# Performance work log

Hardware: AMD Instinct MI355X
Metric: run time of the kernel (lower is better)

The kernel has to match this reference:

```python
import jax, jax.numpy as jnp
import numpy as np

N_NODES = 32768
N_EDGES = 262144
EMB = 64
NUM_HEADS = 4
FEATURE_FDIM = 9
B_MOL = 2048
MAX_PER_MOL = 32


def setup_inputs() -> dict:
    key = jax.random.key(0)
    ks = list(jax.random.split(key, 32))
    nk = lambda: ks.pop()
    inp = {}
    inp['node_feats'] = jax.random.normal(nk(), (N_NODES, FEATURE_FDIM), jnp.float32)
    inp['feature_dist_graph'] = jax.random.normal(nk(), (N_EDGES, FEATURE_FDIM), jnp.float32)
    inp['rij_dist_pairs'] = jax.random.uniform(nk(), (N_EDGES,), jnp.float32)
    see = jax.random.randint(nk(), (N_EDGES, 2), 1, N_NODES + 1, dtype=jnp.int32)
    inp['start_end_env'] = see
    inp['b_scope'] = see[:, 1]  # destination node per edge (index 0 = pad row, never used)
    inp['scope_update'] = jax.random.randint(nk(), (N_EDGES,), 1, N_NODES + 1, dtype=jnp.int32)
    inp['scope_update_lig'] = jax.random.randint(nk(), (N_EDGES,), 1, N_NODES + 1, dtype=jnp.int32)
    inp['l_scope'] = jax.random.randint(nk(), (B_MOL, MAX_PER_MOL), 0, N_NODES + 1, dtype=jnp.int32)
    s = 0.1
    inp['W_emb'] = jax.random.normal(nk(), (FEATURE_FDIM, EMB), jnp.float32) * s
    inp['b_emb'] = jnp.zeros((EMB,), jnp.float32)
    inp['W_dist'] = jax.random.normal(nk(), (FEATURE_FDIM + 1, EMB), jnp.float32) * s
    inp['b_dist'] = jnp.zeros((EMB,), jnp.float32)
    for i in range(NUM_HEADS - 1):
        d = EMB * (i + 1)
        inp[f'fc_W{i}'] = jax.random.normal(nk(), (d, d), jnp.float32) * (1.0 / np.sqrt(d))
        inp[f'fc_b{i}'] = jnp.zeros((d,), jnp.float32)
        inp[f'attn_a{i}'] = jax.random.normal(nk(), (2 * EMB + d, 1), jnp.float32) * s
    return inp


def _segment_attend(logits, vals, seg, num_seg):
    # segment-wise softmax over edges, then weighted scatter-sum to nodes
    m = jax.ops.segment_max(logits, seg, num_segments=num_seg)
    ex = jnp.exp(logits - m[seg])
    den = jax.ops.segment_sum(ex, seg, num_segments=num_seg)
    alpha = ex / den[seg]
    return jax.ops.segment_sum(alpha[:, None] * vals, seg, num_segments=num_seg)


def _forward(node_feats, feature_dist_graph, rij_dist_pairs,
             start_end_env, b_scope, scope_update, scope_update_lig, l_scope,
             W_emb, b_emb, W_dist, b_dist, fc_Ws, fc_bs, attn_as):
    h_orig = node_feats @ W_emb + b_emb                       # [N, EMB]
    h_orig = jnp.concatenate([jnp.zeros((1, EMB), h_orig.dtype), h_orig], axis=0)  # pad row 0
    msg_in = jnp.concatenate([feature_dist_graph, rij_dist_pairs[:, None]], axis=1)
    message = msg_in @ W_dist + b_dist                        # [E, EMB]
    num_seg = h_orig.shape[0]
    tf_feats = h_orig
    for i in range(NUM_HEADS - 1):
        nbr = h_orig[start_end_env]                           # gather: [E, 2, EMB]
        h = message @ fc_Ws[i] + fc_bs[i]                     # [E, D_i]
        logits = jax.nn.leaky_relu(
            jnp.concatenate([nbr[:, 0], nbr[:, 1], h], axis=1) @ attn_as[i],
            negative_slope=0.2)[:, 0]                         # [E]
        out = jax.nn.elu(_segment_attend(logits, h, b_scope, num_seg))  # [N+1, D_i]
        tf_feats = jnp.concatenate([out, h_orig], axis=1)     # merge='cat' -> D_i + EMB
        # updateConnectedDict: rebuild per-edge messages from updated node features
        message = 0.5 * (tf_feats[scope_update_lig] + tf_feats[scope_update])
    cmp_enc = tf_feats[l_scope]                               # [B, P, NUM_HEADS*EMB]
    return cmp_enc.sum(axis=1)                                # [B, NUM_HEADS*EMB]


def reference(node_feats, feature_dist_graph, rij_dist_pairs,
              start_end_env, b_scope, scope_update, scope_update_lig, l_scope,
              W_emb, b_emb, W_dist, b_dist,
              fc_W0, fc_b0, attn_a0, fc_W1, fc_b1, attn_a1, fc_W2, fc_b2, attn_a2):
    return _forward(node_feats, feature_dist_graph, rij_dist_pairs,
                    start_end_env, b_scope, scope_update, scope_update_lig, l_scope,
                    W_emb, b_emb, W_dist, b_dist,
                    [fc_W0, fc_W1, fc_W2], [fc_b0, fc_b1, fc_b2],
                    [attn_a0, attn_a1, attn_a2])
```

## Files before the change

kernel.cpp:

```cpp
#include <hip/hip_runtime.h>
#include <cstdint>
#include <cstddef>

#define NSEG 32769
#define NNODES 32768
#define NE 262144
#define PSZ ((size_t)NSEG * 64)

using f4 = float4;
typedef __attribute__((ext_vector_type(8))) short bf16x8;
typedef __attribute__((ext_vector_type(4))) float f32x4;

__device__ ushort g_tfp[4 * PSZ];
__device__ uint   g_pkA[PSZ];
__device__ uint   g_pk01[PSZ];
__device__ ushort g_msumh[(size_t)NSEG * 192];
__device__ float  g_q[NSEG];
__device__ float  g_p0[3][NSEG];
__device__ float  g_p1[3][NSEG];
__device__ float  g_w2[3][256];
__device__ float  g_wq10[10];
__device__ float  g_cq;
__device__ float  g_wc[640];
__device__ float  g_bcc[64];
__device__ ushort g_wbB[16384];
__device__ ushort g_wbC[36864];
__device__ int    g_counts[NSEG];
__device__ int    g_excl[NSEG];
__device__ int    g_bsum[1024];
__device__ int    g_rowptr[NSEG + 1];
__device__ int    g_cur[NSEG];
__device__ int    g_csr[NE];
__device__ int    g_g1s[NE];
__device__ int    g_g2s[NE];
__device__ float  g_pe1[NE];
__device__ float  g_pe2[NE];
__device__ int    g_bc[128];
__device__ int    g_bcur[128];
__device__ int    g_sorder[NSEG];

#define WREDUCE(x) { x += __shfl_xor(x, 32); x += __shfl_xor(x, 16); \
                     x += __shfl_xor(x, 8);  x += __shfl_xor(x, 4);  \
                     x += __shfl_xor(x, 2);  x += __shfl_xor(x, 1); }
#define WREDMAX(x) { x = fmaxf(x, __shfl_xor(x, 32)); x = fmaxf(x, __shfl_xor(x, 16)); \
                     x = fmaxf(x, __shfl_xor(x, 8));  x = fmaxf(x, __shfl_xor(x, 4));  \
                     x = fmaxf(x, __shfl_xor(x, 2));  x = fmaxf(x, __shfl_xor(x, 1)); }

__device__ __forceinline__ ushort f2bf(float x) {
    uint u = __float_as_uint(x);
    u += 0x7FFF + ((u >> 16) & 1);
    return (ushort)(u >> 16);
}
__device__ __forceinline__ float bfs(ushort u) { return __uint_as_float(((uint)u) << 16); }
__device__ __forceinline__ float bflo(uint u) { return __uint_as_float(u << 16); }
__device__ __forceinline__ float bfhi(uint u) { return __uint_as_float(u & 0xFFFF0000u); }

__global__ __launch_bounds__(256) void k_front(
    const float* __restrict__ node_feats, const float* __restrict__ We,
    const float* __restrict__ be,
    const float* __restrict__ a0, const float* __restrict__ a1, const float* __restrict__ a2,
    const float* __restrict__ W0, const float* __restrict__ W1, const float* __restrict__ W2,
    const float* __restrict__ b0, const float* __restrict__ b1, const float* __restrict__ b2,
    const float* __restrict__ Wd, const float* __restrict__ bd,
    const int* __restrict__ bscope) {
    int tid = threadIdx.x;
    if (blockIdx.x < 513) {
        __shared__ float Ws[576];
        __shared__ float As6[6][68];
        __shared__ float fsAll[576];
        __shared__ float hsAll[64][68];
        int r0 = blockIdx.x * 64;
        for (int i = tid; i < 576; i += 256) Ws[i] = We[i];
        for (int t = tid; t < 384; t += 256) {
            int vec = t >> 6, j = t & 63;
            const float* Av = (vec >> 1) == 0 ? a0 : ((vec >> 1) == 1 ? a1 : a2);
            As6[vec][j] = Av[((vec & 1) << 6) + j];
        }
        for (int t = tid; t < 576; t += 256) {
            int row = r0 + t / 9;
            float v = 0.f;
            if (row >= 1 && row <= NNODES) v = node_feats[(size_t)(row - 1) * 9 + (t % 9)];
            fsAll[t] = v;
        }
        __syncthreads();
        int j = tid & 63;
        float bj = be[j];
#pragma unroll 4
        for (int p = 0; p < 16; p++) {
            int lr = p * 4 + (tid >> 6);
            int row = r0 + lr;
            float acc = bj;
#pragma unroll
            for (int k = 0; k < 9; k++) acc += fsAll[lr * 9 + k] * Ws[k * 64 + j];
            float v = (row == 0 || row >= NSEG) ? 0.f : acc;
            if (row < NSEG) g_tfp[3 * PSZ + (size_t)row * 64 + j] = f2bf(v);
            hsAll[lr][j] = v;
        }
        __syncthreads();
#pragma unroll
        for (int i = 0; i < 12; i++) {
            int task = i * 256 + tid;
            int d = task >> 3, g = tid & 7;
            int lr = d / 6, vec = d % 6;
            float s = 0.f;
#pragma unroll
            for (int jj = 0; jj < 8; jj++)
                s += hsAll[lr][g * 8 + jj] * As6[vec][g * 8 + jj];
            s += __shfl_xor(s, 1); s += __shfl_xor(s, 2); s += __shfl_xor(s, 4);
            int prow = r0 + lr;
            if (g == 0 && prow < NSEG) {
                int iv = vec >> 1;
                if ((vec & 1) == 0) g_p0[iv][prow] = s;
                else                g_p1[iv][prow] = s;
            }
        }
    } else if (blockIdx.x < 518) {
        int pb = blockIdx.x - 513;
        int k = tid;
        if (pb < 3) {
            int it = pb;
            const float* W = it == 0 ? W0 : (it == 1 ? W1 : W2);
            const float* a = it == 0 ? a0 : (it == 1 ? a1 : a2);
            const float* bias = it == 0 ? b0 : (it == 1 ? b1 : b2);
            int d = 64 * (it + 1);
            if (k < d) {
                float s = 0.f;
                for (int jj = 0; jj < d; jj++) s += W[(size_t)k * d + jj] * a[128 + jj];
                g_w2[it][k] = s;
            } else if (k == 255) {
                float c = 0.f;
                for (int jj = 0; jj < d; jj++) c += a[128 + jj] * bias[jj];
                g_w2[it][255] = c;
            }
        } else if (pb == 3) {
            __shared__ float w2s[64];
            if (k < 64) {
                float s = 0.f;
                for (int jj = 0; jj < 64; jj++) s += W0[(size_t)k * 64 + jj] * a0[128 + jj];
                w2s[k] = s;
            }
            __syncthreads();
            if (k < 10) {
                float s = 0.f;
                for (int jj = 0; jj < 64; jj++) s += Wd[(size_t)k * 64 + jj] * w2s[jj];
                g_wq10[k] = s;
            } else if (k == 64) {
                float s = 0.f, c = 0.f;
                for (int jj = 0; jj < 64; jj++) { s += bd[jj] * w2s[jj]; c += a0[128 + jj] * b0[jj]; }
                g_cq = s + c;
            }
        } else {
            for (int t = k; t < 640; t += 256) {
                int kk = t >> 6, jj = t & 63;
                float s = 0.f;
                for (int m = 0; m < 64; m++) s += Wd[kk * 64 + m] * W0[(size_t)m * 64 + jj];
                g_wc[t] = s;
            }
            if (k < 64) {
                float s = b0[k];
                for (int m = 0; m < 64; m++) s += bd[m] * W0[(size_t)m * 64 + k];
                g_bcc[k] = s;
            }
        }
    } else if (blockIdx.x == 518) {
        for (int t = tid; t < 2048; t += 256) {
            int nt = t >> 8, ks = (t >> 6) & 3, l = t & 63;
            int n = nt * 16 + (l & 15);
            int kb = ks * 32 + ((l >> 4) << 3);
            ushort* dst = &g_wbB[(size_t)t * 8];
#pragma unroll
            for (int i = 0; i < 8; i++)
                dst[i] = f2bf(W1[(size_t)(kb + i) * 128 + n]);
        }
    } else if (blockIdx.x <= 520) {
        int half = blockIdx.x - 519;
        for (int t = tid; t < 2304; t += 256) {
            int nt = half * 6 + t / 384;
            int rem = t % 384;
            int ks = rem >> 6, l = rem & 63;
            int n = nt * 16 + (l & 15);
            int kb = ks * 32 + ((l >> 4) << 3);
            ushort* dst = &g_wbC[((size_t)(nt * 6 + ks) * 64 + l) * 8];
#pragma unroll
            for (int i = 0; i < 8; i++)
                dst[i] = f2bf(W2[(size_t)(kb + i) * 192 + n]);
        }
    } else {
        int e = (blockIdx.x - 521) * 256 + tid;
        if (e < NE) atomicAdd(&g_counts[bscope[e]], 1);
    }
}

__global__ void k_scan1() {
    __shared__ int s[256];
    int t = threadIdx.x, i = blockIdx.x * 256 + t;
    int v = (i < NSEG) ? g_counts[i] : 0;
    s[t] = v; __syncthreads();
    for (int off = 1; off < 256; off <<= 1) {
        int tmp = (t >= off) ? s[t - off] : 0;
        __syncthreads();
        s[t] += tmp;
        __syncthreads();
    }
    if (i < NSEG) g_excl[i] = s[t] - v;
    if (t == 255) g_bsum[blockIdx.x] = s[255];
}

__global__ void k_scan2(int nb) {
    __shared__ int s[256];
    int t = threadIdx.x;
    int v = (t < nb) ? g_bsum[t] : 0;
    s[t] = v; __syncthreads();
    for (int off = 1; off < 256; off <<= 1) {
        int tmp = (t >= off) ? s[t - off] : 0;
        __syncthreads();
        s[t] += tmp;
        __syncthreads();
    }
    if (t < nb) g_bsum[t] = s[t] - v;
}

__global__ void k_scan3() {
    __shared__ int lh[128];
    int t = threadIdx.x;
    if (t < 128) lh[t] = 0;
    __syncthreads();
    int i = blockIdx.x * 256 + t;
    if (i < NSEG) {
        g_rowptr[i] = g_excl[i] + g_bsum[i >> 8];
        int cnt = g_counts[i];
        atomicAdd(&lh[cnt > 127 ? 127 : cnt], 1);
    }
    if (i == NSEG) g_rowptr[NSEG] = NE;
    __syncthreads();
    if (t < 128 && lh[t]) atomicAdd(&g_bc[t], lh[t]);
}

__global__ void k_scatter(const int* __restrict__ bs) {
    int e = blockIdx.x * 256 + threadIdx.x;
    if (e < NE) {
        int seg = bs[e];
        int pos = g_rowptr[seg] + atomicAdd(&g_cur[seg], 1);
        g_csr[pos] = e;
    }
}

__global__ __launch_bounds__(256) void k_mid(const int* __restrict__ g1,
                                             const int* __restrict__ g2,
                                             const int* __restrict__ see,
                                             const float* __restrict__ fdg,
                                             const float* __restrict__ rij) {
    int tid = threadIdx.x;
    if (blockIdx.x < 129) {
        __shared__ int sc[128];
        __shared__ int lh[128];
        __shared__ int lbase[128];
        if (tid < 128) { sc[tid] = g_bc[tid]; lh[tid] = 0; }
        __syncthreads();
        for (int off = 1; off < 128; off <<= 1) {
            int tmp = (tid >= off && tid < 128) ? sc[tid - off] : 0;
            __syncthreads();
            if (tid < 128) sc[tid] += tmp;
            __syncthreads();
        }
        int seg = blockIdx.x * 256 + tid;
        int bin = 0, lpos = 0;
        bool valid = seg < NSEG;
        if (valid) {
            int cnt = g_rowptr[seg + 1] - g_rowptr[seg];
            bin = cnt > 127 ? 127 : cnt;
            lpos = atomicAdd(&lh[bin], 1);
        }
        __syncthreads();
        if (tid < 128 && lh[tid] > 0)
            lbase[tid] = atomicAdd(&g_bcur[tid], lh[tid]);
        __syncthreads();
        if (valid) {
            int bstart = sc[bin] - g_bc[bin];
            g_sorder[bstart + lbase[bin] + lpos] = seg;
            g_counts[seg] = 0;
            g_cur[seg] = 0;
        }
    } else if (blockIdx.x < 1153) {
        int pos = (blockIdx.x - 129) * 256 + tid;
        if (pos >= NE) return;
        int e = g_csr[pos];
        g_g1s[pos] = g1[e]; g_g2s[pos] = g2[e];
        int s0 = see[2 * (size_t)e], s1 = see[2 * (size_t)e + 1];
        g_pe1[pos] = g_p0[1][s0] + g_p1[1][s1];
        g_pe2[pos] = g_p0[2][s0] + g_p1[2][s1];
    } else {
        __shared__ float Wcs[640];
        __shared__ float bcs[64];
        __shared__ float wqs[10];
        for (int i = tid; i < 640; i += 256) Wcs[i] = g_wc[i];
        if (tid < 64) bcs[tid] = g_bcc[tid];
        if (tid < 10) wqs[tid] = g_wq10[tid];
        __syncthreads();
        float cq = g_cq;
        int lane = tid & 63;
        int seg = (blockIdx.x - 1153) * 4 + (tid >> 6);
        if (seg >= NSEG) return;
        int beg = g_rowptr[seg], end = g_rowptr[seg + 1];
        int cnt = end - beg;
        float y[10];
#pragma unroll
        for (int k = 0; k < 10; k++) y[k] = 0.f;

        if (cnt > 0 && cnt <= 64) {
            float l = -1e30f;
            float x[10];
#pragma unroll
            for (int k = 0; k < 10; k++) x[k] = 0.f;
            if (lane < cnt) {
                int e = g_csr[beg + lane];
#pragma unroll
                for (int k = 0; k < 9; k++) x[k] = fdg[(size_t)e * 9 + k];
                x[9] = rij[e];
                int s0 = see[2 * (size_t)e], s1 = see[2 * (size_t)e + 1];
                float q = cq;
#pragma unroll
                for (int k = 0; k < 10; k++) q += x[k] * wqs[k];
                l = q + g_p0[0][s0] + g_p1[0][s1];
                l = l > 0.f ? l : 0.2f * l;
            }
            float m = l;
            WREDMAX(m);
            float ex = (lane < cnt) ? __expf(l - m) : 0.f;
            float den = ex;
            WREDUCE(den);
            float w = ex / den;
#pragma unroll
            for (int k = 0; k < 10; k++) {
                float s = w * x[k];
                WREDUCE(s);
                y[k] = s;
            }
        } else if (cnt > 64) {
            float m = -1e30f;
            for (int t = beg + lane; t < end; t += 64) {
                int e = g_csr[t];
                float q = cq;
#pragma unroll
                for (int k = 0; k < 9; k++) q += fdg[(size_t)e * 9 + k] * wqs[k];
                q += rij[e] * wqs[9];
                float l = q + g_p0[0][see[2 * (size_t)e]] + g_p1[0][see[2 * (size_t)e + 1]];
                l = l > 0.f ? l : 0.2f * l;
                m = fmaxf(m, l);
            }
            WREDMAX(m);
            float den = 0.f;
            for (int t = beg + lane; t < end; t += 64) {
                int e = g_csr[t];
                float q = cq;
#pragma unroll
                for (int k = 0; k < 9; k++) q += fdg[(size_t)e * 9 + k] * wqs[k];
                q += rij[e] * wqs[9];
                float l = q + g_p0[0][see[2 * (size_t)e]] + g_p1[0][see[2 * (size_t)e + 1]];
                l = l > 0.f ? l : 0.2f * l;
                den += __expf(l - m);
            }
            WREDUCE(den);
            float rden = 1.f / den;
            float part[10];
#pragma unroll
            for (int k = 0; k < 10; k++) part[k] = 0.f;
            for (int t = beg + lane; t < end; t += 64) {
                int e = g_csr[t];
                float x[10];
#pragma unroll
                for (int k = 0; k < 9; k++) x[k] = fdg[(size_t)e * 9 + k];
                x[9] = rij[e];
                float q = cq;
#pragma unroll
                for (int k = 0; k < 10; k++) q += x[k] * wqs[k];
                float l = q + g_p0[0][see[2 * (size_t)e]] + g_p1[0][see[2 * (size_t)e + 1]];
                l = l > 0.f ? l : 0.2f * l;
                float w = __expf(l - m) * rden;
#pragma unroll
                for (int k = 0; k < 10; k++) part[k] += w * x[k];
            }
#pragma unroll
            for (int k = 0; k < 10; k++) {
                WREDUCE(part[k]);
                y[k] = part[k];
            }
        }
        float o = bcs[lane];
#pragma unroll
        for (int k = 0; k < 10; k++) o += y[k] * Wcs[k * 64 + lane];
        if (cnt == 0) o = 0.f;
        o = o > 0.f ? o : (__expf(o) - 1.f);
        ushort h = g_tfp[3 * PSZ + (size_t)seg * 64 + lane];
        g_pkA[(size_t)seg * 64 + lane] = (uint)f2bf(o) | ((uint)h << 16);
        float qp = o * g_w2[1][lane] + bfs(h) * g_w2[1][64 + lane];
        WREDUCE(qp);
        if (lane == 0) g_q[seg] = qp + g_w2[1][255];
    }
}

template <int NCM>
__global__ __launch_bounds__(256) void k_attendG() {
    const float* __restrict__ pe = (NCM == 2) ? g_pe1 : g_pe2;
    int lane = threadIdx.x & 63;
    int sidx = blockIdx.x * 4 + (threadIdx.x >> 6);
    if (sidx >= NSEG) return;
    int seg = g_sorder[sidx];
    int beg = g_rowptr[seg], end = g_rowptr[seg + 1];
    int cnt = end - beg;
    float acc[NCM];
#pragma unroll
    for (int c = 0; c < NCM; c++) acc[c] = 0.f;

    if (cnt > 0 && cnt <= 64) {
        float l = -1e30f;
        int i1 = 0, i2 = 0;
        if (lane < cnt) {
            i1 = g_g1s[beg + lane]; i2 = g_g2s[beg + lane];
            l = 0.5f * (g_q[i1] + g_q[i2]) + pe[beg + lane];
            l = l > 0.f ? l : 0.2f * l;
        }
        float m = l;
        WREDMAX(m);
        float ex = (lane < cnt) ? __expf(l - m) : 0.f;
        float den = ex;
        WREDUCE(den);
        float w = ex / den;
        for (int t0 = 0; t0 < cnt; t0 += 8) {
            float wt[8]; int a1[8], a2[8];
#pragma unroll
            for (int u = 0; u < 8; u++) {
                int su = t0 + u; su = su > 63 ? 63 : su;
                wt[u] = __shfl(w, su);
                a1[u] = __shfl(i1, su);
                a2[u] = __shfl(i2, su);
            }
            if (NCM == 2) {
                uint ua[8], ub[8];
#pragma unroll
                for (int u = 0; u < 8; u++) {
                    ua[u] = g_pkA[(size_t)a1[u] * 64 + lane];
                    ub[u] = g_pkA[(size_t)a2[u] * 64 + lane];
                }
#pragma unroll
                for (int u = 0; u < 8; u++) {
                    float wh = 0.5f * wt[u];
                    acc[0] += wh * (bflo(ua[u]) + bflo(ub[u]));
                    acc[1] += wh * (bfhi(ua[u]) + bfhi(ub[u]));
                }
            } else {
                uint ua[8], ub[8];
                ushort ha[8], hb[8];
#pragma unroll
                for (int u = 0; u < 8; u++) {
                    size_t b1 = (size_t)a1[u] * 64 + lane, b2 = (size_t)a2[u] * 64 + lane;
                    ua[u] = g_pk01[b1]; ub[u] = g_pk01[b2];
                    ha[u] = g_tfp[3 * PSZ + b1]; hb[u] = g_tfp[3 * PSZ + b2];
                }
#pragma unroll
                for (int u = 0; u < 8; u++) {
                    float wh = 0.5f * wt[u];
                    acc[0] += wh * (bflo(ua[u]) + bflo(ub[u]));
                    acc[1] += wh * (bfhi(ua[u]) + bfhi(ub[u]));
                    acc[2] += wh * (bfs(ha[u]) + bfs(hb[u]));
                }
            }
        }
    } else if (cnt > 64) {
        float m = -1e30f;
        for (int t = beg + lane; t < end; t += 64) {
            float l = 0.5f * (g_q[g_g1s[t]] + g_q[g_g2s[t]]) + pe[t];
            l = l > 0.f ? l : 0.2f * l;
            m = fmaxf(m, l);
        }
        WREDMAX(m);
        float den = 0.f;
        for (int t = beg + lane; t < end; t += 64) {
            float l = 0.5f * (g_q[g_g1s[t]] + g_q[g_g2s[t]]) + pe[t];
            l = l > 0.f ? l : 0.2f * l;
            den += __expf(l - m);
        }
        WREDUCE(den);
        float rden = 1.f / den;
        for (int t = beg; t < end; t++) {
            float l = 0.5f * (g_q[g_g1s[t]] + g_q[g_g2s[t]]) + pe[t];
            l = l > 0.f ? l : 0.2f * l;
            float w = __expf(l - m) * rden;
            float wh = 0.5f * w;
            size_t b1 = (size_t)g_g1s[t] * 64 + lane, b2 = (size_t)g_g2s[t] * 64 + lane;
            if (NCM == 3) {
                uint ua = g_pk01[b1], ub = g_pk01[b2];
                acc[0] += wh * (bflo(ua) + bflo(ub));
                acc[1] += wh * (bfhi(ua) + bfhi(ub));
                acc[2] += wh * (bfs(g_tfp[3 * PSZ + b1]) + bfs(g_tfp[3 * PSZ + b2]));
            } else {
                uint ua = g_pkA[b1], ub = g_pkA[b2];
                acc[0] += wh * (bflo(ua) + bflo(ub));
                acc[1] += wh * (bfhi(ua) + bfhi(ub));
            }
        }
    }
#pragma unroll
    for (int c = 0; c < NCM; c++)
        g_msumh[(size_t)seg * 192 + lane + 64 * c] = f2bf(acc[c]);
}

__global__ __launch_bounds__(256) void k_gemmB(const float* __restrict__ bias) {
    int tid = threadIdx.x;
    if (blockIdx.x == 0 && tid < 128) { g_bc[tid] = 0; g_bcur[tid] = 0; }
    int w = tid >> 6, l = tid & 63;
    int lm = l & 15, lk = l >> 4;
    int r0 = blockIdx.x * 64 + w * 16;
    int arow = r0 + lm;
    size_t abase = (size_t)(arow < NSEG ? arow : 0) * 192;
    f32x4 acc[8];
#pragma unroll
    for (int nt = 0; nt < 8; nt++) acc[nt] = (f32x4){0.f, 0.f, 0.f, 0.f};
#pragma unroll
    for (int ks = 0; ks < 4; ks++) {
        bf16x8 af = *(const bf16x8*)&g_msumh[abase + ks * 32 + lk * 8];
#pragma unroll
        for (int nt = 0; nt < 8; nt++) {
            bf16x8 bf = *(const bf16x8*)&g_wbB[((size_t)(nt * 4 + ks) * 64 + l) * 8];
            acc[nt] = __builtin_amdgcn_mfma_f32_16x16x32_bf16(af, bf, acc[nt], 0, 0, 0);
        }
    }
#pragma unroll
    for (int j = 0; j < 4; j++) {
        int row = r0 + lk * 4 + j;
        bool valid = row < NSEG;
        int rr = valid ? row : 0;
        bool nonempty = valid && (g_rowptr[row + 1] > g_rowptr[row]);
        float qp = 0.f;
#pragma unroll
        for (int nt = 0; nt < 4; nt++) {
            int c = nt * 16 + lm;
            float vl = acc[nt][j] + bias[c];
            float vh = acc[nt + 4][j] + bias[64 + c];
            if (!nonempty) { vl = 0.f; vh = 0.f; }
            vl = vl > 0.f ? vl : (__expf(vl) - 1.f);
            vh = vh > 0.f ? vh : (__expf(vh) - 1.f);
            float hc = bfs(g_tfp[3 * PSZ + (size_t)rr * 64 + c]);
            if (valid) g_pk01[(size_t)row * 64 + c] = (uint)f2bf(vl) | ((uint)f2bf(vh) << 16);
            qp += vl * g_w2[2][c] + vh * g_w2[2][64 + c] + hc * g_w2[2][128 + c];
        }
        qp += __shfl_xor(qp, 1); qp += __shfl_xor(qp, 2);
        qp += __shfl_xor(qp, 4); qp += __shfl_xor(qp, 8);
        if (valid && lm == 0) g_q[row] = qp + g_w2[2][255];
    }
}

__global__ __launch_bounds__(256) void k_gemmC(const float* __restrict__ bias) {
    int tid = threadIdx.x;
    int w = tid >> 6, l = tid & 63;
    int lm = l & 15, lk = l >> 4;
    int r0 = blockIdx.x * 64 + w * 16;
    int arow = r0 + lm;
    size_t abase = (size_t)(arow < NSEG ? arow : 0) * 192;
    f32x4 acc[12];
#pragma unroll
    for (int nt = 0; nt < 12; nt++) acc[nt] = (f32x4){0.f, 0.f, 0.f, 0.f};
#pragma unroll
    for (int ks = 0; ks < 6; ks++) {
        bf16x8 af = *(const bf16x8*)&g_msumh[abase + ks * 32 + lk * 8];
#pragma unroll
        for (int nt = 0; nt < 12; nt++) {
            bf16x8 bf = *(const bf16x8*)&g_wbC[((size_t)(nt * 6 + ks) * 64 + l) * 8];
            acc[nt] = __builtin_amdgcn_mfma_f32_16x16x32_bf16(af, bf, acc[nt], 0, 0, 0);
        }
    }
#pragma unroll
    for (int j = 0; j < 4; j++) {
        int row = r0 + lk * 4 + j;
        if (row >= NSEG) continue;
        bool nonempty = g_rowptr[row + 1] > g_rowptr[row];
#pragma unroll
        for (int nt = 0; nt < 12; nt++) {
            int col = nt * 16 + lm;
            float v = acc[nt][j] + bias[col];
            if (!nonempty) v = 0.f;
            v = v > 0.f ? v : (__expf(v) - 1.f);
            int plane = nt >> 2, c = col & 63;
            g_tfp[(size_t)plane * PSZ + (size_t)row * 64 + c] = f2bf(v);
        }
    }
}

__global__ void k_final(const int* __restrict__ lscope, float* __restrict__ out) {
    __shared__ int idx[32];
    __shared__ float sm[4][256];
    int m = blockIdx.x, tid = threadIdx.x, w = tid >> 6, lane = tid & 63;
    if (tid < 32) idx[tid] = lscope[m * 32 + tid];
    __syncthreads();
    float a0 = 0.f, a1 = 0.f, a2 = 0.f, a3 = 0.f;
#pragma unroll
    for (int j = w * 8; j < w * 8 + 8; j++) {
        size_t base = (size_t)idx[j] * 64 + lane;
        a0 += bfs(g_tfp[base]);
        a1 += bfs(g_tfp[PSZ + base]);
        a2 += bfs(g_tfp[2 * PSZ + base]);
        a3 += bfs(g_tfp[3 * PSZ + base]);
    }
    sm[w][lane] = a0; sm[w][64 + lane] = a1; sm[w][128 + lane] = a2; sm[w][192 + lane] = a3;
    __syncthreads();
    out[(size_t)m * 256 + tid] = sm[0][tid] + sm[1][tid] + sm[2][tid] + sm[3][tid];
}

extern "C" void kernel_launch(void* const* d_in, const int* in_sizes, int n_in,
                              void* d_out, int out_size, void* d_ws, size_t ws_size,
                              hipStream_t stream) {
    const float* node_feats = (const float*)d_in[0];
    const float* fdg        = (const float*)d_in[1];
    const float* rij        = (const float*)d_in[2];
    const int*   see        = (const int*)d_in[3];
    const int*   b_scope    = (const int*)d_in[4];
    const int*   scope_up   = (const int*)d_in[5];
    const int*   scope_lig  = (const int*)d_in[6];
    const int*   l_scope    = (const int*)d_in[7];
    const float* W_emb      = (const float*)d_in[8];
    const float* b_emb      = (const float*)d_in[9];
    const float* W_dist     = (const float*)d_in[10];
    const float* b_dist     = (const float*)d_in[11];
    const float* fc_W[3]   = {(const float*)d_in[12], (const float*)d_in[15], (const float*)d_in[18]};
    const float* fc_b[3]   = {(const float*)d_in[13], (const float*)d_in[16], (const float*)d_in[19]};
    const float* attn_a[3] = {(const float*)d_in[14], (const float*)d_in[17], (const float*)d_in[20]};

    k_front<<<1545, 256, 0, stream>>>(node_feats, W_emb, b_emb,
                                      attn_a[0], attn_a[1], attn_a[2],
                                      fc_W[0], fc_W[1], fc_W[2],
                                      fc_b[0], fc_b[1], fc_b[2],
                                      W_dist, b_dist, b_scope);
    k_scan1<<<129, 256, 0, stream>>>();
    k_scan2<<<1, 256, 0, stream>>>(129);
    k_scan3<<<129, 256, 0, stream>>>();
    k_scatter<<<NE / 256, 256, 0, stream>>>(b_scope);
    k_mid<<<9346, 256, 0, stream>>>(scope_lig, scope_up, see, fdg, rij);

    k_attendG<2><<<8193, 256, 0, stream>>>();
    k_gemmB<<<513, 256, 0, stream>>>(fc_b[1]);
    k_attendG<3><<<8193, 256, 0, stream>>>();
    k_gemmC<<<513, 256, 0, stream>>>(fc_b[2]);

    k_final<<<2048, 256, 0, stream>>>(l_scope, (float*)d_out);
}
```

Before: 207.8 us.

## Precompute per-edge records in scatter kernel for coalesced gathers in k_mid

The scatter kernel now also reads each edge's features, distance, endpoint projections and scope indices in original edge order, computes the layer-0 attention logit, and writes a packed 64-byte float4 record per edge. k_mid then gathers these records through the CSR permutation with vector loads, instead of doing scattered 9-float feature reads and projection lookups, and no longer recomputes the logit in each pass over large segments. The cost is an extra 16 MB write plus a later read of the record buffer, with the gathers still random by edge id.

Result: no change. 203.8 us (median of 2 runs) (-1.9%).

```diff
diff --git a/kernel.cpp b/kernel.cpp
--- a/kernel.cpp
+++ b/kernel.cpp
@@ -25,6 +25,7 @@
 __device__ float  g_bcc[64];
 __device__ ushort g_wbB[16384];
 __device__ ushort g_wbC[36864];
+__device__ f4     g_rec[(size_t)NE * 4];
 __device__ int    g_counts[NSEG];
 __device__ int    g_excl[NSEG];
 __device__ int    g_bsum[1024];
@@ -236,20 +237,39 @@
     if (t < 128 && lh[t]) atomicAdd(&g_bc[t], lh[t]);
 }
 
-__global__ void k_scatter(const int* __restrict__ bs) {
+__global__ __launch_bounds__(256) void k_scatter(const int* __restrict__ bs,
+                                                 const float* __restrict__ fdg,
+                                                 const float* __restrict__ rij,
+                                                 const int* __restrict__ see,
+                                                 const int* __restrict__ g1,
+                                                 const int* __restrict__ g2) {
+    __shared__ float wqs[10];
+    if (threadIdx.x < 10) wqs[threadIdx.x] = g_wq10[threadIdx.x];
+    __syncthreads();
     int e = blockIdx.x * 256 + threadIdx.x;
-    if (e < NE) {
-        int seg = bs[e];
-        int pos = g_rowptr[seg] + atomicAdd(&g_cur[seg], 1);
-        g_csr[pos] = e;
-    }
-}
-
-__global__ __launch_bounds__(256) void k_mid(const int* __restrict__ g1,
-                                             const int* __restrict__ g2,
-                                             const int* __restrict__ see,
-                                             const float* __restrict__ fdg,
-                                             const float* __restrict__ rij) {
+    if (e >= NE) return;
+    int seg = bs[e];
+    int pos = g_rowptr[seg] + atomicAdd(&g_cur[seg], 1);
+    g_csr[pos] = e;
+    float x[10];
+#pragma unroll
+    for (int k = 0; k < 9; k++) x[k] = fdg[(size_t)e * 9 + k];
+    x[9] = rij[e];
+    int s0 = see[2 * (size_t)e], s1 = see[2 * (size_t)e + 1];
+    float q = g_cq;
+#pragma unroll
+    for (int k = 0; k < 10; k++) q += x[k] * wqs[k];
+    float lb0 = q + g_p0[0][s0] + g_p1[0][s1];
+    float pe1 = g_p0[1][s0] + g_p1[1][s1];
+    float pe2 = g_p0[2][s0] + g_p1[2][s1];
+    size_t rb = (size_t)e * 4;
+    g_rec[rb + 0] = make_float4(x[0], x[1], x[2], x[3]);
+    g_rec[rb + 1] = make_float4(x[4], x[5], x[6], x[7]);
+    g_rec[rb + 2] = make_float4(x[8], x[9], lb0, 0.f);
+    g_rec[rb + 3] = make_float4(pe1, pe2, __int_as_float(g1[e]), __int_as_float(g2[e]));
+}
+
+__global__ __launch_bounds__(256) void k_mid() {
     int tid = threadIdx.x;
     if (blockIdx.x < 129) {
         __shared__ int sc[128];
@@ -285,19 +305,17 @@
         int pos = (blockIdx.x - 129) * 256 + tid;
         if (pos >= NE) return;
         int e = g_csr[pos];
-        g_g1s[pos] = g1[e]; g_g2s[pos] = g2[e];
-        int s0 = see[2 * (size_t)e], s1 = see[2 * (size_t)e + 1];
-        g_pe1[pos] = g_p0[1][s0] + g_p1[1][s1];
-        g_pe2[pos] = g_p0[2][s0] + g_p1[2][s1];
+        f4 d = g_rec[(size_t)e * 4 + 3];
+        g_pe1[pos] = d.x;
+        g_pe2[pos] = d.y;
+        g_g1s[pos] = __float_as_int(d.z);
+        g_g2s[pos] = __float_as_int(d.w);
     } else {
         __shared__ float Wcs[640];
         __shared__ float bcs[64];
-        __shared__ float wqs[10];
         for (int i = tid; i < 640; i += 256) Wcs[i] = g_wc[i];
         if (tid < 64) bcs[tid] = g_bcc[tid];
-        if (tid < 10) wqs[tid] = g_wq10[tid];
-        __syncthreads();
-        float cq = g_cq;
+        __syncthreads();
         int lane = tid & 63;
         int seg = (blockIdx.x - 1153) * 4 + (tid >> 6);
         if (seg >= NSEG) return;
@@ -314,14 +332,14 @@
             for (int k = 0; k < 10; k++) x[k] = 0.f;
             if (lane < cnt) {
                 int e = g_csr[beg + lane];
-#pragma unroll
-                for (int k = 0; k < 9; k++) x[k] = fdg[(size_t)e * 9 + k];
-                x[9] = rij[e];
-                int s0 = see[2 * (size_t)e], s1 = see[2 * (size_t)e + 1];
-                float q = cq;
-#pragma unroll
-                for (int k = 0; k < 10; k++) q += x[k] * wqs[k];
-                l = q + g_p0[0][s0] + g_p1[0][s1];
+                size_t rb = (size_t)e * 4;
+                f4 r0 = g_rec[rb + 0];
+                f4 r1 = g_rec[rb + 1];
+                f4 r2 = g_rec[rb + 2];
+                x[0] = r0.x; x[1] = r0.y; x[2] = r0.z; x[3] = r0.w;
+                x[4] = r1.x; x[5] = r1.y; x[6] = r1.z; x[7] = r1.w;
+                x[8] = r2.x; x[9] = r2.y;
+                l = r2.z;
                 l = l > 0.f ? l : 0.2f * l;
             }
             float m = l;
@@ -340,11 +358,7 @@
             float m = -1e30f;
             for (int t = beg + lane; t < end; t += 64) {
                 int e = g_csr[t];
-                float q = cq;
-#pragma unroll
-                for (int k = 0; k < 9; k++) q += fdg[(size_t)e * 9 + k] * wqs[k];
-                q += rij[e] * wqs[9];
-                float l = q + g_p0[0][see[2 * (size_t)e]] + g_p1[0][see[2 * (size_t)e + 1]];
+                float l = g_rec[(size_t)e * 4 + 2].z;
                 l = l > 0.f ? l : 0.2f * l;
                 m = fmaxf(m, l);
             }
@@ -352,11 +366,7 @@
             float den = 0.f;
             for (int t = beg + lane; t < end; t += 64) {
                 int e = g_csr[t];
-                float q = cq;
-#pragma unroll
-                for (int k = 0; k < 9; k++) q += fdg[(size_t)e * 9 + k] * wqs[k];
-                q += rij[e] * wqs[9];
-                float l = q + g_p0[0][see[2 * (size_t)e]] + g_p1[0][see[2 * (size_t)e + 1]];
+                float l = g_rec[(size_t)e * 4 + 2].z;
                 l = l > 0.f ? l : 0.2f * l;
                 den += __expf(l - m);
             }
@@ -367,18 +377,16 @@
             for (int k = 0; k < 10; k++) part[k] = 0.f;
             for (int t = beg + lane; t < end; t += 64) {
                 int e = g_csr[t];
-                float x[10];
-#pragma unroll
-                for (int k = 0; k < 9; k++) x[k] = fdg[(size_t)e * 9 + k];
-                x[9] = rij[e];
-                float q = cq;
-#pragma unroll
-                for (int k = 0; k < 10; k++) q += x[k] * wqs[k];
-                float l = q + g_p0[0][see[2 * (size_t)e]] + g_p1[0][see[2 * (size_t)e + 1]];
+                size_t rb = (size_t)e * 4;
+                f4 r0 = g_rec[rb + 0];
+                f4 r1 = g_rec[rb + 1];
+                f4 r2 = g_rec[rb + 2];
+                float l = r2.z;
                 l = l > 0.f ? l : 0.2f * l;
                 float w = __expf(l - m) * rden;
-#pragma unroll
-                for (int k = 0; k < 10; k++) part[k] += w * x[k];
+                part[0] += w * r0.x; part[1] += w * r0.y; part[2] += w * r0.z; part[3] += w * r0.w;
+                part[4] += w * r1.x; part[5] += w * r1.y; part[6] += w * r1.z; part[7] += w * r1.w;
+                part[8] += w * r2.x; part[9] += w * r2.y;
             }
 #pragma unroll
             for (int k = 0; k < 10; k++) {
@@ -633,8 +641,8 @@
     k_scan1<<<129, 256, 0, stream>>>();
     k_scan2<<<1, 256, 0, stream>>>(129);
     k_scan3<<<129, 256, 0, stream>>>();
-    k_scatter<<<NE / 256, 256, 0, stream>>>(b_scope);
-    k_mid<<<9346, 256, 0, stream>>>(scope_lig, scope_up, see, fdg, rij);
+    k_scatter<<<NE / 256, 256, 0, stream>>>(b_scope, fdg, rij, see, scope_lig, scope_up);
+    k_mid<<<9346, 256, 0, stream>>>();
 
     k_attendG<2><<<8193, 256, 0, stream>>>();
     k_gemmB<<<513, 256, 0, stream>>>(fc_b[1]);
```
